# Optimization experiments

Hardware: AMD Instinct MI355X
Metric: run time of the kernel (lower is better)

Reference implementation:

```python
import jax, jax.numpy as jnp
import numpy as np

N_FFT = 400          # Whisper n_fft
HOP = 160            # Whisper hop_length
CUT = N_FFT // 2 + 1 # freq_cutoff = 201
T_SIG = 9_600_000    # 10 minutes @ 16 kHz


def _make_basis():
    # fourier_basis[k, n] = exp(-2*pi*i*k*n/N); keep first CUT rows,
    # stack [real; imag], multiply by periodic Hann window.
    n = jnp.arange(N_FFT, dtype=jnp.float32)
    k = jnp.arange(CUT, dtype=jnp.float32)
    ang = (2.0 * jnp.pi / N_FFT) * k[:, None] * n[None, :]          # [CUT, N_FFT]
    window = 0.5 * (1.0 - jnp.cos(2.0 * jnp.pi * n / N_FFT))        # periodic Hann
    basis = jnp.concatenate([jnp.cos(ang), -jnp.sin(ang)], axis=0)  # [2*CUT, N_FFT]
    return (basis * window[None, :]).astype(jnp.float32)


def setup_inputs() -> dict:
    key = jax.random.key(0)
    signal = jax.random.normal(key, (T_SIG,), dtype=jnp.float32)
    basis = _make_basis()  # conv weight, exact DFT basis (frozen in original)
    return {"signal": signal, "basis": basis}


def reference(signal, basis):
    # zero-pad by freq_cutoff-1 on each side, then strided conv == windowed DFT
    pad = CUT - 1
    x = jnp.pad(signal, (pad, pad))[None, None, :]          # [1, 1, T+2*pad]
    w = basis[:, None, :]                                    # [2*CUT, 1, N_FFT]
    y = jax.lax.conv_general_dilated(
        x, w, window_strides=(HOP,), padding='VALID',
        dimension_numbers=('NCH', 'OIH', 'NCH'))             # [1, 2*CUT, frames]
    real = y[:, :CUT, :]
    imag = y[:, CUT:2 * CUT, :]
    return real, imag
```

## Files before the change

kernel.cpp:

```cpp
#include <hip/hip_runtime.h>

#define HOP 160
#define NROWS 402
#define NTAPS 400
#define T_SIG 9600000
#define N_FRAMES 60001
#define PAD 200

typedef __bf16 bf16x8 __attribute__((ext_vector_type(8)));
typedef float f32x16 __attribute__((ext_vector_type(16)));
typedef unsigned short u16x8 __attribute__((ext_vector_type(8)));
typedef unsigned short u16x4 __attribute__((ext_vector_type(4)));
typedef unsigned int u32x4 __attribute__((ext_vector_type(4)));

__device__ __forceinline__ unsigned short f2bf(float f) {
    unsigned int u = __builtin_bit_cast(unsigned int, f);
    u += 0x7fffu + ((u >> 16) & 1u);
    return (unsigned short)(u >> 16);
}

__device__ __forceinline__ void gll16(const void* g, void* l) {
    __builtin_amdgcn_global_load_lds(
        (const __attribute__((address_space(1))) unsigned int*)g,
        (__attribute__((address_space(3))) unsigned int*)l, 16, 0, 0);
}


#define SIG_OFF 425984
#define APH0 0
#define APH1 28672
#define APH2 57344
#define APH3 81920
#define ABM_STRIDE 106496
#define A_LDS_B 30720
#define SIG_LDS_B 45056
#define NEED1 (425984UL + 20172800UL)

__global__ void prep_sig(const float* __restrict__ sig,
                         unsigned short* __restrict__ sp) {
    long chunk = (long)blockIdx.x * 256 + threadIdx.x;
    if (chunk >= 2401440L) return;
    long i = chunk * 4;
    long pos = i + 8 * (i / 160);
    u16x4 v;
    if (i >= 200 && i + 4 <= 9600200L) {
        float4 f = *reinterpret_cast<const float4*>(sig + (i - 200));
        v[0] = f2bf(f.x); v[1] = f2bf(f.y); v[2] = f2bf(f.z); v[3] = f2bf(f.w);
    } else {
        v[0] = v[1] = v[2] = v[3] = 0;
    }
    *reinterpret_cast<u16x4*>(sp + pos) = v;
}

__global__ void prep_a(const float* __restrict__ basis,
                       unsigned short* __restrict__ ap) {
    int s = blockIdx.x * 256 + threadIdx.x;
    int bm = s / 6656, rem = s % 6656;
    int sip, kb;
    if (rem < 1792)      { sip = rem;        kb = 0;  }
    else if (rem < 3584) { sip = rem - 1792; kb = 7;  }
    else if (rem < 5120) { sip = rem - 3584; kb = 14; }
    else                 { sip = rem - 5120; kb = 20; }
    int ksg = sip >> 7, r = sip & 127;
    int ka = kb + (ksg >> 1);
    int k0 = ka * 16 + (ksg & 1) * 8;
    int m = bm * 128 + r;
    u16x8 v;
#pragma unroll
    for (int j = 0; j < 8; ++j) {
        int k = k0 + j;
        float f = (m < NROWS && k < NTAPS) ? basis[m * NTAPS + k] : 0.0f;
        v[j] = f2bf(f);
    }
    *reinterpret_cast<u16x8*>(ap + (size_t)s * 8) = v;
}

#define A_LOAD(POFF, N) do { _Pragma("unroll") \
    for (int it = 0; it < (N); ++it) { \
        int slot = it * 256 + tid; \
        areg[it] = *reinterpret_cast<const u32x4*>(aBase + (POFF) + slot * 16); \
    } } while (0)

#define A_WRITE(N) do { _Pragma("unroll") \
    for (int it = 0; it < (N); ++it) { \
        int slot = it * 256 + tid; \
        *reinterpret_cast<u32x4*>(aB + (slot & 127) * 240 + (slot >> 7) * 16) = areg[it]; \
    } } while (0)

#define COMPUTE_PHASE(KSB, KSN) do { _Pragma("unroll") \
    for (int i = 0; i < (KSN); ++i) { \
        const int ka = (KSB) + i; \
        const int sc = ka * 32 + (ka >= 10 ? 16 : 0) + (ka >= 20 ? 16 : 0); \
        bf16x8 a0 = *reinterpret_cast<const bf16x8*>(aR0g + i * 32); \
        bf16x8 a1 = *reinterpret_cast<const bf16x8*>(aR0g + 7680 + i * 32); \
        bf16x8 b0 = *reinterpret_cast<const bf16x8*>(sB0 + sc); \
        bf16x8 b1 = *reinterpret_cast<const bf16x8*>(sB0 + 10752 + sc); \
        acc00 = __builtin_amdgcn_mfma_f32_32x32x16_bf16(a0, b0, acc00, 0, 0, 0); \
        acc01 = __builtin_amdgcn_mfma_f32_32x32x16_bf16(a0, b1, acc01, 0, 0, 0); \
        acc10 = __builtin_amdgcn_mfma_f32_32x32x16_bf16(a1, b0, acc10, 0, 0, 0); \
        acc11 = __builtin_amdgcn_mfma_f32_32x32x16_bf16(a1, b1, acc11, 0, 0, 0); \
    } } while (0)

#define STORE_ACC(A, R0, T) do { if ((T) < (long)N_FRAMES) { _Pragma("unroll") \
    for (int r = 0; r < 16; ++r) { \
        int row = (R0) + (r & 3) + 8 * (r >> 2); \
        if (row < NROWS) out[(long)row * N_FRAMES + (T)] = (A)[r]; \
    } } } while (0)

__launch_bounds__(256)
__global__ void stft_gemm(const unsigned short* __restrict__ sigp,
                          const unsigned short* __restrict__ apack,
                          float* __restrict__ out) {
    __shared__ __align__(16) char lds[A_LDS_B + SIG_LDS_B];
    char* aB = lds;
    char* sB = lds + A_LDS_B;
    const int tid = threadIdx.x;
    const int bm = blockIdx.x & 3;
    const int bt = blockIdx.x >> 2;
    const char* aBase = (const char*)apack + (size_t)bm * ABM_STRIDE;

    u32x4 areg[7];
    A_LOAD(APH0, 7);
    {
        const char* sg = (const char*)sigp + (size_t)bt * 43008;
#pragma unroll
        for (int it = 0; it < 11; ++it) {
            int slot = it * 256 + tid;
            gll16(sg + slot * 16, sB + slot * 16);
        }
    }
    A_WRITE(7);
    __syncthreads();

    const int lane = tid & 63;
    const int w = tid >> 6;
    const int wm = w >> 1;
    const int wf = w & 1;
    const int l31 = lane & 31;
    const int g = lane >> 5;

    const char* aR0g = aB + (wm * 64 + l31) * 240 + g * 16;
    const char* sB0 = sB + (wf * 64 + l31) * 336 + g * 16;

    f32x16 acc00 = {0,0,0,0,0,0,0,0,0,0,0,0,0,0,0,0};
    f32x16 acc01 = {0,0,0,0,0,0,0,0,0,0,0,0,0,0,0,0};
    f32x16 acc10 = {0,0,0,0,0,0,0,0,0,0,0,0,0,0,0,0};
    f32x16 acc11 = {0,0,0,0,0,0,0,0,0,0,0,0,0,0,0,0};

    A_LOAD(APH1, 7);
    COMPUTE_PHASE(0, 7);
    __syncthreads();
    A_WRITE(7);
    __syncthreads();

    A_LOAD(APH2, 6);
    COMPUTE_PHASE(7, 7);
    __syncthreads();
    A_WRITE(6);
    __syncthreads();

    A_LOAD(APH3, 6);
    COMPUTE_PHASE(14, 6);
    __syncthreads();
    A_WRITE(6);
    __syncthreads();

    COMPUTE_PHASE(20, 6);

    const int rBase = bm * 128 + wm * 64 + 4 * g;
    const long tBase = (long)bt * 128 + wf * 64 + l31;
    STORE_ACC(acc00, rBase, tBase);
    STORE_ACC(acc01, rBase, tBase + 32);
    STORE_ACC(acc10, rBase + 32, tBase);
    STORE_ACC(acc11, rBase + 32, tBase + 32);
}

#define MT 13
#define KS 26
#define FPB 128
#define MSPLIT 3
#define NBT ((N_FRAMES + FPB - 1) / FPB)
#define SPAN (127*HOP + 416)
#define SPAN4 (SPAN/4)
#define LDSE 21776

__global__ void stft_prep2(const float* __restrict__ basis,
                           unsigned short* __restrict__ packed) {
    int tid = blockIdx.x * 256 + threadIdx.x;
    if (tid >= MT * KS * 64) return;
    int lane = tid & 63;
    int frag = tid >> 6;
    int ks = frag % KS;
    int mt = frag / KS;
    int row = mt * 32 + (lane & 31);
    int colb = ks * 16 + (lane >> 5) * 8;
    u16x8 v;
#pragma unroll
    for (int i = 0; i < 8; ++i) {
        int col = colb + i;
        float f = (row < NROWS && col < NTAPS) ? basis[row * NTAPS + col] : 0.0f;
        v[i] = f2bf(f);
    }
    *reinterpret_cast<u16x8*>(packed + (size_t)tid * 8) = v;
}

__launch_bounds__(256, 3)
__global__ void stft_mfma2(const float* __restrict__ sig,
                           const unsigned short* __restrict__ packedA,
                           float* __restrict__ out) {
    __shared__ unsigned short sl[LDSE];
    const int tid = threadIdx.x;
    const int bt = blockIdx.x % NBT;
    const int bmm = blockIdx.x / NBT;
    const long sbase = (long)bt * (FPB * HOP) - PAD;
    for (int idx = tid; idx < SPAN4; idx += 256) {
        const int e = idx * 4;
        const long g0 = sbase + e;
        float4 v;
        if (g0 >= 0 && g0 + 4 <= (long)T_SIG) {
            v = *reinterpret_cast<const float4*>(sig + g0);
        } else {
            v.x = (g0 + 0 >= 0 && g0 + 0 < (long)T_SIG) ? sig[g0 + 0] : 0.0f;
            v.y = (g0 + 1 >= 0 && g0 + 1 < (long)T_SIG) ? sig[g0 + 1] : 0.0f;
            v.z = (g0 + 2 >= 0 && g0 + 2 < (long)T_SIG) ? sig[g0 + 2] : 0.0f;
            v.w = (g0 + 3 >= 0 && g0 + 3 < (long)T_SIG) ? sig[g0 + 3] : 0.0f;
        }
        u16x4 s;
        s[0] = f2bf(v.x); s[1] = f2bf(v.y); s[2] = f2bf(v.z); s[3] = f2bf(v.w);
        const int pos = e + 8 * (e / 160);
        *reinterpret_cast<u16x4*>(&sl[pos]) = s;
    }
    __syncthreads();
    const int lane = tid & 63;
    const int w = tid >> 6;
    const int l31 = lane & 31;
    const int g = lane >> 5;
    const int lf = w * 32 + l31;
    const long t = (long)bt * FPB + lf;
    const int mt0 = (bmm == 0) ? 0 : 5 + 4 * (bmm - 1);
    const int mtN = (bmm == 0) ? 5 : 4;
    const unsigned short* bbase = &sl[lf * 168 + g * 8];
    const int rowg = 4 * g;
#pragma unroll 1
    for (int mi = 0; mi < mtN; ++mi) {
        const int mt = mt0 + mi;
        f32x16 acc = {0,0,0,0,0,0,0,0,0,0,0,0,0,0,0,0};
        const unsigned short* pA = packedA + ((size_t)(mt * KS) * 64 + lane) * 8;
#pragma unroll
        for (int ks = 0; ks < KS; ++ks) {
            const bf16x8 a = *reinterpret_cast<const bf16x8*>(pA + (size_t)ks * 512);
            const bf16x8 b = *reinterpret_cast<const bf16x8*>(bbase + ks * 16 + 8 * (ks / 10));
            acc = __builtin_amdgcn_mfma_f32_32x32x16_bf16(a, b, acc, 0, 0, 0);
        }
        if (t < N_FRAMES) {
            const int rb = mt * 32 + rowg;
#pragma unroll
            for (int r = 0; r < 16; ++r) {
                const int row = rb + (r & 3) + 8 * (r >> 2);
                if (row < NROWS) out[(long)row * N_FRAMES + t] = acc[r];
            }
        }
        __syncthreads();
    }
}

__global__ void stft_naive(const float* __restrict__ sig,
                           const float* __restrict__ basis,
                           float* __restrict__ out) {
    long idx = (long)blockIdx.x * 256 + threadIdx.x;
    if (idx >= (long)NROWS * N_FRAMES) return;
    int row = (int)(idx / N_FRAMES);
    int tt = (int)(idx % N_FRAMES);
    long s0 = (long)tt * HOP - PAD;
    float acc = 0.0f;
    for (int n = 0; n < NTAPS; ++n) {
        long s = s0 + n;
        float x = (s >= 0 && s < (long)T_SIG) ? sig[s] : 0.0f;
        acc = fmaf(x, basis[row * NTAPS + n], acc);
    }
    out[idx] = acc;
}

extern "C" void kernel_launch(void* const* d_in, const int* in_sizes, int n_in,
                              void* d_out, int out_size, void* d_ws, size_t ws_size,
                              hipStream_t stream) {
    (void)in_sizes; (void)n_in; (void)out_size;
    const float* sig = (const float*)d_in[0];
    const float* basis = (const float*)d_in[1];
    float* out = (float*)d_out;
    if (ws_size >= NEED1) {
        unsigned short* ap = (unsigned short*)d_ws;
        unsigned short* sp = (unsigned short*)((char*)d_ws + SIG_OFF);
        prep_sig<<<9381, 256, 0, stream>>>(sig, sp);
        prep_a<<<104, 256, 0, stream>>>(basis, ap);
        stft_gemm<<<469 * 4, 256, 0, stream>>>(sp, ap, out);
    } else if (ws_size >= (size_t)MT * KS * 64 * 8 * sizeof(unsigned short)) {
        unsigned short* packed = (unsigned short*)d_ws;
        stft_prep2<<<(MT * KS * 64 + 255) / 256, 256, 0, stream>>>(basis, packed);
        stft_mfma2<<<NBT * MSPLIT, 256, 0, stream>>>(sig, packed, out);
    } else {
        long total = (long)NROWS * N_FRAMES;
        stft_naive<<<(int)((total + 255) / 256), 256, 0, stream>>>(sig, basis, out);
    }
}
```

Before: 67.78 us.

## Stream basis through small LDS buffer in 13 two-kstep phases to shrink LDS

Restructures the GEMM's A-operand (DFT basis) staging. Instead of four large phases holding about 30 KB of basis in LDS, it streams 13 small phases of two k-steps each through a 9 KB buffer with a 72-byte row stride, and repacks the prep kernel to match. Signal LDS is also trimmed and the load is guarded. The block index mapping now puts frame tiles first rather than basis row tiles. Smaller LDS and fewer registers should allow more blocks per CU, at the cost of many more __syncthreads barriers and less compute between them.

New measurement: 99.83 us. 47.3% more time.

```diff
diff --git a/kernel.cpp b/kernel.cpp
--- a/kernel.cpp
+++ b/kernel.cpp
@@ -27,13 +27,9 @@
 
 
 #define SIG_OFF 425984
-#define APH0 0
-#define APH1 28672
-#define APH2 57344
-#define APH3 81920
 #define ABM_STRIDE 106496
-#define A_LDS_B 30720
-#define SIG_LDS_B 45056
+#define SIG_LDS_B 43552
+#define A_LDS_B 9216
 #define NEED1 (425984UL + 20172800UL)
 
 __global__ void prep_sig(const float* __restrict__ sig,
@@ -56,14 +52,10 @@
                        unsigned short* __restrict__ ap) {
     int s = blockIdx.x * 256 + threadIdx.x;
     int bm = s / 6656, rem = s % 6656;
-    int sip, kb;
-    if (rem < 1792)      { sip = rem;        kb = 0;  }
-    else if (rem < 3584) { sip = rem - 1792; kb = 7;  }
-    else if (rem < 5120) { sip = rem - 3584; kb = 14; }
-    else                 { sip = rem - 5120; kb = 20; }
-    int ksg = sip >> 7, r = sip & 127;
-    int ka = kb + (ksg >> 1);
-    int k0 = ka * 16 + (ksg & 1) * 8;
+    int p = rem >> 9, s2 = rem & 511;
+    int r = s2 >> 2, q = s2 & 3;
+    int ka = 2 * p + (q >> 1);
+    int k0 = ka * 16 + (q & 1) * 8;
     int m = bm * 128 + r;
     u16x8 v;
 #pragma unroll
@@ -74,32 +66,6 @@
     }
     *reinterpret_cast<u16x8*>(ap + (size_t)s * 8) = v;
 }
-
-#define A_LOAD(POFF, N) do { _Pragma("unroll") \
-    for (int it = 0; it < (N); ++it) { \
-        int slot = it * 256 + tid; \
-        areg[it] = *reinterpret_cast<const u32x4*>(aBase + (POFF) + slot * 16); \
-    } } while (0)
-
-#define A_WRITE(N) do { _Pragma("unroll") \
-    for (int it = 0; it < (N); ++it) { \
-        int slot = it * 256 + tid; \
-        *reinterpret_cast<u32x4*>(aB + (slot & 127) * 240 + (slot >> 7) * 16) = areg[it]; \
-    } } while (0)
-
-#define COMPUTE_PHASE(KSB, KSN) do { _Pragma("unroll") \
-    for (int i = 0; i < (KSN); ++i) { \
-        const int ka = (KSB) + i; \
-        const int sc = ka * 32 + (ka >= 10 ? 16 : 0) + (ka >= 20 ? 16 : 0); \
-        bf16x8 a0 = *reinterpret_cast<const bf16x8*>(aR0g + i * 32); \
-        bf16x8 a1 = *reinterpret_cast<const bf16x8*>(aR0g + 7680 + i * 32); \
-        bf16x8 b0 = *reinterpret_cast<const bf16x8*>(sB0 + sc); \
-        bf16x8 b1 = *reinterpret_cast<const bf16x8*>(sB0 + 10752 + sc); \
-        acc00 = __builtin_amdgcn_mfma_f32_32x32x16_bf16(a0, b0, acc00, 0, 0, 0); \
-        acc01 = __builtin_amdgcn_mfma_f32_32x32x16_bf16(a0, b1, acc01, 0, 0, 0); \
-        acc10 = __builtin_amdgcn_mfma_f32_32x32x16_bf16(a1, b0, acc10, 0, 0, 0); \
-        acc11 = __builtin_amdgcn_mfma_f32_32x32x16_bf16(a1, b1, acc11, 0, 0, 0); \
-    } } while (0)
 
 #define STORE_ACC(A, R0, T) do { if ((T) < (long)N_FRAMES) { _Pragma("unroll") \
     for (int r = 0; r < 16; ++r) { \
@@ -111,25 +77,30 @@
 __global__ void stft_gemm(const unsigned short* __restrict__ sigp,
                           const unsigned short* __restrict__ apack,
                           float* __restrict__ out) {
-    __shared__ __align__(16) char lds[A_LDS_B + SIG_LDS_B];
-    char* aB = lds;
-    char* sB = lds + A_LDS_B;
+    __shared__ __align__(16) char lds[SIG_LDS_B + A_LDS_B];
+    char* sB = lds;
+    char* aB = lds + SIG_LDS_B;
     const int tid = threadIdx.x;
-    const int bm = blockIdx.x & 3;
-    const int bt = blockIdx.x >> 2;
+    const int bt = blockIdx.x % 469;
+    const int bm = blockIdx.x / 469;
     const char* aBase = (const char*)apack + (size_t)bm * ABM_STRIDE;
 
-    u32x4 areg[7];
-    A_LOAD(APH0, 7);
+    u32x4 areg0, areg1;
+    areg0 = *reinterpret_cast<const u32x4*>(aBase + (size_t)tid * 16);
+    areg1 = *reinterpret_cast<const u32x4*>(aBase + (size_t)(256 + tid) * 16);
     {
         const char* sg = (const char*)sigp + (size_t)bt * 43008;
 #pragma unroll
         for (int it = 0; it < 11; ++it) {
             int slot = it * 256 + tid;
-            gll16(sg + slot * 16, sB + slot * 16);
-        }
-    }
-    A_WRITE(7);
+            if (slot < 2722) gll16(sg + slot * 16, sB + slot * 16);
+        }
+    }
+    {
+        int s0 = tid, s1 = 256 + tid;
+        *reinterpret_cast<u32x4*>(aB + (s0 >> 2) * 72 + (s0 & 3) * 16) = areg0;
+        *reinterpret_cast<u32x4*>(aB + (s1 >> 2) * 72 + (s1 & 3) * 16) = areg1;
+    }
     __syncthreads();
 
     const int lane = tid & 63;
@@ -139,7 +110,7 @@
     const int l31 = lane & 31;
     const int g = lane >> 5;
 
-    const char* aR0g = aB + (wm * 64 + l31) * 240 + g * 16;
+    const char* aR = aB + (wm * 64 + l31) * 72 + g * 16;
     const char* sB0 = sB + (wf * 64 + l31) * 336 + g * 16;
 
     f32x16 acc00 = {0,0,0,0,0,0,0,0,0,0,0,0,0,0,0,0};
@@ -147,25 +118,34 @@
     f32x16 acc10 = {0,0,0,0,0,0,0,0,0,0,0,0,0,0,0,0};
     f32x16 acc11 = {0,0,0,0,0,0,0,0,0,0,0,0,0,0,0,0};
 
-    A_LOAD(APH1, 7);
-    COMPUTE_PHASE(0, 7);
-    __syncthreads();
-    A_WRITE(7);
-    __syncthreads();
-
-    A_LOAD(APH2, 6);
-    COMPUTE_PHASE(7, 7);
-    __syncthreads();
-    A_WRITE(6);
-    __syncthreads();
-
-    A_LOAD(APH3, 6);
-    COMPUTE_PHASE(14, 6);
-    __syncthreads();
-    A_WRITE(6);
-    __syncthreads();
-
-    COMPUTE_PHASE(20, 6);
+#pragma unroll
+    for (int p = 0; p < 13; ++p) {
+        if (p < 12) {
+            const char* nb = aBase + (size_t)(p + 1) * 8192;
+            areg0 = *reinterpret_cast<const u32x4*>(nb + (size_t)tid * 16);
+            areg1 = *reinterpret_cast<const u32x4*>(nb + (size_t)(256 + tid) * 16);
+        }
+#pragma unroll
+        for (int kl = 0; kl < 2; ++kl) {
+            const int ka = 2 * p + kl;
+            const int sc = ka * 32 + (ka >= 10 ? 16 : 0) + (ka >= 20 ? 16 : 0);
+            bf16x8 a0 = *reinterpret_cast<const bf16x8*>(aR + kl * 32);
+            bf16x8 a1 = *reinterpret_cast<const bf16x8*>(aR + 2304 + kl * 32);
+            bf16x8 b0 = *reinterpret_cast<const bf16x8*>(sB0 + sc);
+            bf16x8 b1 = *reinterpret_cast<const bf16x8*>(sB0 + 10752 + sc);
+            acc00 = __builtin_amdgcn_mfma_f32_32x32x16_bf16(a0, b0, acc00, 0, 0, 0);
+            acc01 = __builtin_amdgcn_mfma_f32_32x32x16_bf16(a0, b1, acc01, 0, 0, 0);
+            acc10 = __builtin_amdgcn_mfma_f32_32x32x16_bf16(a1, b0, acc10, 0, 0, 0);
+            acc11 = __builtin_amdgcn_mfma_f32_32x32x16_bf16(a1, b1, acc11, 0, 0, 0);
+        }
+        __syncthreads();
+        if (p < 12) {
+            int s0 = tid, s1 = 256 + tid;
+            *reinterpret_cast<u32x4*>(aB + (s0 >> 2) * 72 + (s0 & 3) * 16) = areg0;
+            *reinterpret_cast<u32x4*>(aB + (s1 >> 2) * 72 + (s1 & 3) * 16) = areg1;
+            __syncthreads();
+        }
+    }
 
     const int rBase = bm * 128 + wm * 64 + 4 * g;
     const long tBase = (long)bt * 128 + wf * 64 + l31;
```
